# Performance work log

Measured on AMD Instinct MI355X. Metric: run time of the kernel, lower is better.

## Reference

```python
import jax, jax.numpy as jnp
import numpy as np

BLOCK_SIZE = 64  # weights per (scale, zero_point) block along in_features


def _dequant(q_weights, q_scales, q_zp):
    # q_weights: [N, K] int codes in [0,16); q_scales/q_zp: [N, K//BLOCK_SIZE]
    N, K = q_weights.shape
    nb = K // BLOCK_SIZE
    q = q_weights.reshape(N, nb, BLOCK_SIZE).astype(q_scales.dtype)
    zp = q_zp.reshape(N, nb, 1).astype(q_scales.dtype)
    s = q_scales.reshape(N, nb, 1)
    return ((q - zp) * s).reshape(N, K)  # [N, K] float


def setup_inputs() -> dict:
    key = jax.random.key(0)
    k1, k2, k3, k4, k5 = jax.random.split(key, 5)
    M, K, N = 4096, 4096, 11008
    nb = K // BLOCK_SIZE
    return {
        "input": jax.random.normal(k1, (M, K), dtype=jnp.float32),
        "q_weights": jax.random.randint(k2, (N, K), 0, 16, dtype=jnp.int32),
        "q_scales": jax.random.uniform(k3, (N, nb), dtype=jnp.float32, minval=0.01, maxval=0.05),
        "q_zp": jax.random.randint(k4, (N, nb), 0, 16, dtype=jnp.int32),
        "bias": jax.random.normal(k5, (N,), dtype=jnp.float32),
    }


def reference(input, q_weights, q_scales, q_zp, bias):
    # Blockwise int4 dequant + GEMM: out[m, n] = sum_k input[m, k] * w[n, k]
    w = _dequant(q_weights, q_scales, q_zp)          # [N, K]
    out = jnp.einsum("mk,nk->mn", input, w)          # [M, N]
    return out + bias[None, :]
```

## Files before the change

### kernel.cpp

```cpp
#include <hip/hip_runtime.h>


#define BM 128
#define BN 128
#define BK 64
#define LDSN 72

typedef __attribute__((ext_vector_type(8))) short bf16x8;
typedef __attribute__((ext_vector_type(4))) float f32x4;

__device__ __forceinline__ unsigned short f2bf(float f) {
    union { float f; unsigned int u; } v; v.f = f;
    unsigned int u = v.u;
    u += 0x7FFFu + ((u >> 16) & 1u);
    return (unsigned short)(u >> 16);
}
__device__ __forceinline__ unsigned int pack2(float a, float b) {
    return (unsigned int)f2bf(a) | ((unsigned int)f2bf(b) << 16);
}

__device__ __forceinline__ void gl_lds16(const void* gp, void* lp) {
    __builtin_amdgcn_global_load_lds(
        (const __attribute__((address_space(1))) unsigned int*)gp,
        (__attribute__((address_space(3))) unsigned int*)lp,
        16, 0, 0);
}

__device__ __forceinline__ unsigned lds_off(const void* p) {
    return (unsigned)(unsigned long long)
        (const __attribute__((address_space(3))) void*)p;
}

template<int IMM>
__device__ __forceinline__ bf16x8 ds128(unsigned a) {
    bf16x8 d;
    asm volatile("ds_read_b128 %0, %1 offset:%2"
                 : "=v"(d) : "v"(a), "i"(IMM));
    return d;
}

__global__ __launch_bounds__(256)
void prep_kernel(const float* __restrict__ A, const int* __restrict__ Q,
                 const float* __restrict__ S, const int* __restrict__ Zp,
                 unsigned short* __restrict__ Ab, unsigned short* __restrict__ W,
                 int M, int K, int nb)
{
    const int y = blockIdx.y;
    const int k = (blockIdx.x * 256 + threadIdx.x) * 8;
    if (k >= K) return;
    if (y < M) {
        const float4* ap = (const float4*)(A + (size_t)y * K + k);
        float4 a0 = ap[0], a1 = ap[1];
        uint4 o;
        o.x = pack2(a0.x, a0.y); o.y = pack2(a0.z, a0.w);
        o.z = pack2(a1.x, a1.y); o.w = pack2(a1.z, a1.w);
        *(uint4*)(Ab + (size_t)y * K + k) = o;
    } else {
        const int n = y - M;
        const int kb = k >> 6;
        const float s  = S[(size_t)n * nb + kb];
        const float zs = (float)Zp[(size_t)n * nb + kb] * s;
        const int4* qp = (const int4*)(Q + (size_t)n * K + k);
        int4 q0 = qp[0], q1 = qp[1];
        uint4 o;
        o.x = pack2((float)q0.x * s - zs, (float)q0.y * s - zs);
        o.y = pack2((float)q0.z * s - zs, (float)q0.w * s - zs);
        o.z = pack2((float)q1.x * s - zs, (float)q1.y * s - zs);
        o.w = pack2((float)q1.z * s - zs, (float)q1.w * s - zs);
        *(uint4*)(W + (size_t)n * K + k) = o;
    }
}


#define G8_BARRIER() asm volatile("s_barrier" ::: "memory")
#define G8_VMCNT(n)  asm volatile("s_waitcnt vmcnt(" #n ")" ::: "memory")
#define G8_LGKMC(n)  asm volatile("s_waitcnt lgkmcnt(" #n ")" ::: "memory")
#define G8_LGKM0()   do { asm volatile("s_waitcnt lgkmcnt(0)" ::: "memory"); \
    __builtin_amdgcn_sched_barrier(0); } while (0)

#define G8_STAGE(G, kt, h, base, b)                                          \
  do {                                                                       \
    const unsigned short* _s = (G) + (long)(kt) * 64 + (long)(h) * 128 * K;  \
    gl_lds16(_s + aoff0, (base) + (b) * 32768 + (h) * 16384 + lds0);         \
    gl_lds16(_s + aoff1, (base) + (b) * 32768 + (h) * 16384 + lds1);         \
  } while (0)

#define G8_LOAD_AF(b, mh)                                                    \
  af[0][0] = ds128<(b)*32768 + (mh)*16384 + 0*2048>(pA0);                    \
  af[1][0] = ds128<(b)*32768 + (mh)*16384 + 1*2048>(pA0);                    \
  af[2][0] = ds128<(b)*32768 + (mh)*16384 + 2*2048>(pA0);                    \
  af[3][0] = ds128<(b)*32768 + (mh)*16384 + 3*2048>(pA0);                    \
  af[0][1] = ds128<(b)*32768 + (mh)*16384 + 0*2048>(pA1);                    \
  af[1][1] = ds128<(b)*32768 + (mh)*16384 + 1*2048>(pA1);                    \
  af[2][1] = ds128<(b)*32768 + (mh)*16384 + 2*2048>(pA1);                    \
  af[3][1] = ds128<(b)*32768 + (mh)*16384 + 3*2048>(pA1);

#define G8_LOAD_BF(b, nh, BF)                                                \
  BF[0][0] = ds128<(b)*32768 + (nh)*16384 + 0*2048>(pB0);                    \
  BF[1][0] = ds128<(b)*32768 + (nh)*16384 + 1*2048>(pB0);                    \
  BF[0][1] = ds128<(b)*32768 + (nh)*16384 + 0*2048>(pB1);                    \
  BF[1][1] = ds128<(b)*32768 + (nh)*16384 + 1*2048>(pB1);

#define G8_MFMA(q, BF)                                                       \
  __builtin_amdgcn_s_setprio(1);                                             \
  { _Pragma("unroll") for (int _i = 0; _i < 4; ++_i)                         \
    _Pragma("unroll") for (int _j = 0; _j < 2; ++_j) {                       \
      acc[q][_i][_j] = __builtin_amdgcn_mfma_f32_16x16x32_bf16(              \
          af[_i][0], BF[_j][0], acc[q][_i][_j], 0, 0, 0);                    \
      acc[q][_i][_j] = __builtin_amdgcn_mfma_f32_16x16x32_bf16(              \
          af[_i][1], BF[_j][1], acc[q][_i][_j], 0, 0, 0);                    \
  } }                                                                        \
  __builtin_amdgcn_s_setprio(0);

__global__ __launch_bounds__(512, 2)
void gemm8_kernel(const unsigned short* __restrict__ Ab,
                  const unsigned short* __restrict__ Wb,
                  const float* __restrict__ bias, float* __restrict__ C,
                  int M, int N, int K)
{
    __shared__ __align__(16) unsigned short As[2][256][64];
    __shared__ __align__(16) unsigned short Bs[2][256][64];

    const int tid  = threadIdx.x;

    const int nwg = gridDim.x;
    int wg = blockIdx.x;
    {
        const int q8 = nwg >> 3, r8 = nwg & 7, x = wg & 7, s = wg >> 3;
        wg = (x < r8 ? x * (q8 + 1) : r8 * (q8 + 1) + (x - r8) * q8) + s;
    }
    const int gx = M / 256;
    const int m0 = (wg % gx) * 256;
    const int n0 = (wg / gx) * 256;

    const int lane = tid & 63;
    const int wave = tid >> 6;
    const int ww   = wave >> 2;
    const int wv   = wave & 3;
    const int fr   = lane & 15;
    const int quad = lane >> 4;
    const int sw   = fr & 7;

    const int rl0 = tid >> 3;
    const int rl1 = (512 + tid) >> 3;
    const int pp  = tid & 7;
    const long aoff0 = (long)rl0 * K + (long)((pp ^ (rl0 & 7)) * 8);
    const long aoff1 = (long)rl1 * K + (long)((pp ^ (rl1 & 7)) * 8);
    const int lds0 = tid * 16;
    const int lds1 = (512 + tid) * 16;

    const int ck0 = ((quad    ) ^ sw) * 16;
    const int ck1 = ((quad + 4) ^ sw) * 16;
    const int arow = ww * 64 + fr;
    const int brow = wv * 32 + fr;

    char* AsB = (char*)&As[0][0][0];
    char* BsB = (char*)&Bs[0][0][0];
    const unsigned pA0 = lds_off(AsB) + arow * 128 + ck0;
    const unsigned pA1 = lds_off(AsB) + arow * 128 + ck1;
    const unsigned pB0 = lds_off(BsB) + brow * 128 + ck0;
    const unsigned pB1 = lds_off(BsB) + brow * 128 + ck1;

    const unsigned short* Ag = Ab + (size_t)m0 * K;
    const unsigned short* Bg = Wb + (size_t)n0 * K;

    f32x4 acc[4][4][2];
    #pragma unroll
    for (int q = 0; q < 4; ++q)
        #pragma unroll
        for (int i = 0; i < 4; ++i)
            #pragma unroll
            for (int j = 0; j < 2; ++j)
                acc[q][i][j] = (f32x4){0.f, 0.f, 0.f, 0.f};

    bf16x8 af[4][2], bf0[2][2], bf1[2][2];

    G8_STAGE(Ag, 0, 0, AsB, 0);
    G8_STAGE(Bg, 0, 0, BsB, 0);
    G8_STAGE(Ag, 0, 1, AsB, 0);
    G8_STAGE(Bg, 0, 1, BsB, 0);
    G8_STAGE(Ag, 1, 0, AsB, 1);
    G8_STAGE(Bg, 1, 0, BsB, 1);
    G8_VMCNT(4);
    G8_BARRIER();

    const int nit = K / 128;
    for (int it = 0; it < nit - 1; ++it) {
        const int t = 2 * it;
        G8_LOAD_AF(0, 0) G8_LOAD_BF(0, 0, bf0)
        G8_STAGE(Ag, t + 1, 1, AsB, 1);
        G8_LGKMC(8);
        G8_BARRIER(); G8_LGKM0();
        G8_MFMA(0, bf0);
        G8_VMCNT(6);
        G8_BARRIER();
        G8_LOAD_BF(0, 1, bf1)
        G8_STAGE(Bg, t + 1, 1, BsB, 1);
        G8_BARRIER(); G8_LGKM0();
        G8_MFMA(1, bf1);
        G8_BARRIER();
        G8_LOAD_AF(0, 1)
        G8_STAGE(Ag, t + 2, 0, AsB, 0);
        G8_BARRIER(); G8_LGKM0();
        G8_MFMA(2, bf0);
        G8_BARRIER();
        G8_STAGE(Bg, t + 2, 0, BsB, 0);
        G8_BARRIER();
        G8_MFMA(3, bf1);
        G8_VMCNT(8);
        G8_BARRIER();
        G8_LOAD_AF(1, 0) G8_LOAD_BF(1, 0, bf0)
        G8_STAGE(Ag, t + 2, 1, AsB, 0);
        G8_LGKMC(8);
        G8_BARRIER(); G8_LGKM0();
        G8_MFMA(0, bf0);
        G8_VMCNT(6);
        G8_BARRIER();
        G8_LOAD_BF(1, 1, bf1)
        G8_STAGE(Bg, t + 2, 1, BsB, 0);
        G8_BARRIER(); G8_LGKM0();
        G8_MFMA(1, bf1);
        G8_BARRIER();
        G8_LOAD_AF(1, 1)
        G8_STAGE(Ag, t + 3, 0, AsB, 1);
        G8_BARRIER(); G8_LGKM0();
        G8_MFMA(2, bf0);
        G8_BARRIER();
        G8_STAGE(Bg, t + 3, 0, BsB, 1);
        G8_BARRIER();
        G8_MFMA(3, bf1);
        G8_VMCNT(8);
        G8_BARRIER();
    }
    {
        G8_LOAD_AF(0, 0) G8_LOAD_BF(0, 0, bf0)
        G8_STAGE(Ag, 2 * nit - 1, 1, AsB, 1);
        G8_LGKMC(8);
        G8_BARRIER(); G8_LGKM0(); G8_MFMA(0, bf0); G8_VMCNT(6); G8_BARRIER();

        G8_LOAD_BF(0, 1, bf1)
        G8_STAGE(Bg, 2 * nit - 1, 1, BsB, 1);
        G8_BARRIER(); G8_LGKM0(); G8_MFMA(1, bf1); G8_BARRIER();

        G8_LOAD_AF(0, 1)
        G8_BARRIER(); G8_LGKM0(); G8_MFMA(2, bf0); G8_BARRIER();

        G8_BARRIER(); G8_MFMA(3, bf1); G8_VMCNT(4); G8_BARRIER();

        G8_LOAD_AF(1, 0) G8_LOAD_BF(1, 0, bf0)
        G8_BARRIER(); G8_LGKM0(); G8_MFMA(0, bf0); G8_VMCNT(0); G8_BARRIER();

        G8_LOAD_BF(1, 1, bf1)
        G8_BARRIER(); G8_LGKM0(); G8_MFMA(1, bf1); G8_BARRIER();

        G8_LOAD_AF(1, 1)
        G8_BARRIER(); G8_LGKM0(); G8_MFMA(2, bf0); G8_BARRIER();

        G8_MFMA(3, bf1);
    }

    #pragma unroll
    for (int q = 0; q < 4; ++q) {
        const int mh = q >> 1, nh = q & 1;
        #pragma unroll
        for (int j = 0; j < 2; ++j) {
            const int n = n0 + nh * 128 + brow + j * 16;
            const float bv = bias[n];
            #pragma unroll
            for (int i = 0; i < 4; ++i) {
                const int mb = m0 + mh * 128 + ww * 64 + i * 16 + quad * 4;
                #pragma unroll
                for (int r = 0; r < 4; ++r)
                    C[(size_t)(mb + r) * N + n] = acc[q][i][j][r] + bv;
            }
        }
    }
}

__global__ __launch_bounds__(256, 2)
void gemm_bt_kernel(const unsigned short* __restrict__ Ab,
                    const unsigned short* __restrict__ Wb,
                    const float* __restrict__ bias, float* __restrict__ C,
                    int M, int N, int K)
{
    __shared__ __align__(16) unsigned short As[BM * BK];
    __shared__ __align__(16) unsigned short Bs[BN * BK];

    const int tid = threadIdx.x;
    const int m0  = blockIdx.x * BM;
    const int n0  = blockIdx.y * BN;

    const int lane = tid & 63;
    const int wave = tid >> 6;
    const int wm   = (wave >> 1) * 64;
    const int wn   = (wave & 1) * 64;
    const int fr   = lane & 15;
    const int quad = lane >> 4;
    const int sw   = fr & 7;

    f32x4 acc[4][4];
    #pragma unroll
    for (int i = 0; i < 4; ++i)
        #pragma unroll
        for (int j = 0; j < 4; ++j)
            acc[i][j] = (f32x4){0.f, 0.f, 0.f, 0.f};

    const int ktiles = K / BK;
    for (int kt = 0; kt < ktiles; ++kt) {
        const int k0 = kt * BK;
        #pragma unroll
        for (int i = 0; i < 4; ++i) {
            const int c    = i * 256 + tid;
            const int row  = c >> 3;
            const int g    = (c & 7) ^ (row & 7);
            const int cole = g * 8;
            gl_lds16(Ab + (size_t)(m0 + row) * K + k0 + cole, (char*)As + c * 16);
            gl_lds16(Wb + (size_t)(n0 + row) * K + k0 + cole, (char*)Bs + c * 16);
        }
        __syncthreads();

        #pragma unroll
        for (int ks = 0; ks < 2; ++ks) {
            bf16x8 af[4], bfg[4];
            #pragma unroll
            for (int i = 0; i < 4; ++i) {
                const int row = wm + i * 16 + fr;
                const int p   = (ks * 4 + quad) ^ sw;
                af[i] = *(const bf16x8*)&As[row * BK + p * 8];
            }
            #pragma unroll
            for (int j = 0; j < 4; ++j) {
                const int row = wn + j * 16 + fr;
                const int p   = (ks * 4 + quad) ^ sw;
                bfg[j] = *(const bf16x8*)&Bs[row * BK + p * 8];
            }
            #pragma unroll
            for (int i = 0; i < 4; ++i)
                #pragma unroll
                for (int j = 0; j < 4; ++j)
                    acc[i][j] = __builtin_amdgcn_mfma_f32_16x16x32_bf16(af[i], bfg[j], acc[i][j], 0, 0, 0);
        }
        __syncthreads();
    }

    #pragma unroll
    for (int j = 0; j < 4; ++j) {
        const int n = n0 + wn + j * 16 + fr;
        const float bv = bias[n];
        #pragma unroll
        for (int i = 0; i < 4; ++i) {
            const int mb = m0 + wm + i * 16 + quad * 4;
            #pragma unroll
            for (int r = 0; r < 4; ++r)
                C[(size_t)(mb + r) * N + n] = acc[i][j][r] + bv;
        }
    }
}

__global__ __launch_bounds__(256, 2)
void q4gemm_fused(const float* __restrict__ A, const int* __restrict__ Q,
                  const float* __restrict__ S, const int* __restrict__ Zp,
                  const float* __restrict__ bias, float* __restrict__ C,
                  int M, int N, int K, int nb)
{
    __shared__ __align__(16) unsigned short As[BM * LDSN];
    __shared__ __align__(16) unsigned short Bs[BN * LDSN];

    const int tid = threadIdx.x;
    const int m0  = blockIdx.x * BM;
    const int n0  = blockIdx.y * BN;
    const int srow = tid >> 4;
    const int scol = (tid & 15) << 2;
    const int lane = tid & 63;
    const int wave = tid >> 6;
    const int wm   = (wave >> 1) * 64;
    const int wn   = (wave & 1) * 64;
    const int fr   = lane & 15;
    const int quad = lane >> 4;

    f32x4 acc[4][4];
    #pragma unroll
    for (int i = 0; i < 4; ++i)
        #pragma unroll
        for (int j = 0; j < 4; ++j)
            acc[i][j] = (f32x4){0.f, 0.f, 0.f, 0.f};

    const int ktiles = K / BK;
    for (int kt = 0; kt < ktiles; ++kt) {
        const int k0 = kt * BK;
        #pragma unroll
        for (int i = 0; i < 8; ++i) {
            const int r = i * 16 + srow;
            const float4 v = *(const float4*)(A + (size_t)(m0 + r) * K + k0 + scol);
            uint2 p; p.x = pack2(v.x, v.y); p.y = pack2(v.z, v.w);
            *(uint2*)&As[r * LDSN + scol] = p;
        }
        #pragma unroll
        for (int i = 0; i < 8; ++i) {
            const int r = i * 16 + srow;
            const int n = n0 + r;
            const int4 q = *(const int4*)(Q + (size_t)n * K + k0 + scol);
            const float s  = S[(size_t)n * nb + kt];
            const float zs = (float)Zp[(size_t)n * nb + kt] * s;
            uint2 p;
            p.x = pack2((float)q.x * s - zs, (float)q.y * s - zs);
            p.y = pack2((float)q.z * s - zs, (float)q.w * s - zs);
            *(uint2*)&Bs[r * LDSN + scol] = p;
        }
        __syncthreads();
        #pragma unroll
        for (int ks = 0; ks < 2; ++ks) {
            bf16x8 af[4], bfg[4];
            #pragma unroll
            for (int i = 0; i < 4; ++i)
                af[i] = *(const bf16x8*)&As[(wm + i * 16 + fr) * LDSN + ks * 32 + quad * 8];
            #pragma unroll
            for (int j = 0; j < 4; ++j)
                bfg[j] = *(const bf16x8*)&Bs[(wn + j * 16 + fr) * LDSN + ks * 32 + quad * 8];
            #pragma unroll
            for (int i = 0; i < 4; ++i)
                #pragma unroll
                for (int j = 0; j < 4; ++j)
                    acc[i][j] = __builtin_amdgcn_mfma_f32_16x16x32_bf16(af[i], bfg[j], acc[i][j], 0, 0, 0);
        }
        __syncthreads();
    }
    #pragma unroll
    for (int j = 0; j < 4; ++j) {
        const int n = n0 + wn + j * 16 + fr;
        const float bv = bias[n];
        #pragma unroll
        for (int i = 0; i < 4; ++i) {
            const int mb = m0 + wm + i * 16 + quad * 4;
            #pragma unroll
            for (int r = 0; r < 4; ++r)
                C[(size_t)(mb + r) * N + n] = acc[i][j][r] + bv;
        }
    }
}

extern "C" void kernel_launch(void* const* d_in, const int* in_sizes, int n_in,
                              void* d_out, int out_size, void* d_ws, size_t ws_size,
                              hipStream_t stream) {
    const float* A    = (const float*)d_in[0];
    const int*   Q    = (const int*)d_in[1];
    const float* S    = (const float*)d_in[2];
    const int*   Zp   = (const int*)d_in[3];
    const float* bias = (const float*)d_in[4];
    float* C = (float*)d_out;

    const int N  = in_sizes[4];
    const int K  = in_sizes[1] / N;
    const int M  = in_sizes[0] / K;
    const int nb = in_sizes[2] / N;

    const size_t needA = (size_t)M * K * 2;
    const size_t needW = (size_t)N * K * 2;

    if (ws_size >= needA + needW && (K % 2048) == 0) {
        unsigned short* Ab = (unsigned short*)d_ws;
        unsigned short* Wb = (unsigned short*)((char*)d_ws + needA);

        dim3 pgrid(K / 2048, M + N);
        prep_kernel<<<pgrid, 256, 0, stream>>>(A, Q, S, Zp, Ab, Wb, M, K, nb);

        if ((M % 256) == 0 && (N % 256) == 0 && (K % 128) == 0 && K >= 256) {
            gemm8_kernel<<<dim3((M / 256) * (N / 256)), dim3(512), 0, stream>>>(
                Ab, Wb, bias, C, M, N, K);
        } else {
            dim3 grid(M / BM, N / BN);
            gemm_bt_kernel<<<grid, dim3(256), 0, stream>>>(Ab, Wb, bias, C, M, N, K);
        }
    } else {
        dim3 grid(M / BM, N / BN);
        q4gemm_fused<<<grid, dim3(256), 0, stream>>>(A, Q, S, Zp, bias, C, M, N, K, nb);
    }
}
```

Baseline: 654.2 us.

## Double-buffer A fragments and prefetch LDS reads ahead of MFMA phases

Adds a second A-fragment register set so LDS reads for the next quadrant are issued before the current MFMA block runs. Partial lgkmcnt waits replace the full waits and a barrier before each MFMA phase, so LDS latency overlaps with matrix math. The prologue, the main loop and the tail are rescheduled to match, and the launch guard now requires K to be a multiple of 256. The extra fragment registers raise VGPR pressure under the 512-thread, 2-blocks-per-CU launch bound.

```diff
diff --git a/kernel.cpp b/kernel.cpp
--- a/kernel.cpp
+++ b/kernel.cpp
@@ -74,8 +74,7 @@
 
 #define G8_BARRIER() asm volatile("s_barrier" ::: "memory")
 #define G8_VMCNT(n)  asm volatile("s_waitcnt vmcnt(" #n ")" ::: "memory")
-#define G8_LGKMC(n)  asm volatile("s_waitcnt lgkmcnt(" #n ")" ::: "memory")
-#define G8_LGKM0()   do { asm volatile("s_waitcnt lgkmcnt(0)" ::: "memory"); \
+#define G8_LGKMC(n)  do { asm volatile("s_waitcnt lgkmcnt(" #n ")" ::: "memory"); \
     __builtin_amdgcn_sched_barrier(0); } while (0)
 
 #define G8_STAGE(G, kt, h, base, b)                                          \
@@ -85,15 +84,15 @@
     gl_lds16(_s + aoff1, (base) + (b) * 32768 + (h) * 16384 + lds1);         \
   } while (0)
 
-#define G8_LOAD_AF(b, mh)                                                    \
-  af[0][0] = ds128<(b)*32768 + (mh)*16384 + 0*2048>(pA0);                    \
-  af[1][0] = ds128<(b)*32768 + (mh)*16384 + 1*2048>(pA0);                    \
-  af[2][0] = ds128<(b)*32768 + (mh)*16384 + 2*2048>(pA0);                    \
-  af[3][0] = ds128<(b)*32768 + (mh)*16384 + 3*2048>(pA0);                    \
-  af[0][1] = ds128<(b)*32768 + (mh)*16384 + 0*2048>(pA1);                    \
-  af[1][1] = ds128<(b)*32768 + (mh)*16384 + 1*2048>(pA1);                    \
-  af[2][1] = ds128<(b)*32768 + (mh)*16384 + 2*2048>(pA1);                    \
-  af[3][1] = ds128<(b)*32768 + (mh)*16384 + 3*2048>(pA1);
+#define G8_LOAD_AF(b, mh, AF)                                                \
+  AF[0][0] = ds128<(b)*32768 + (mh)*16384 + 0*2048>(pA0);                    \
+  AF[1][0] = ds128<(b)*32768 + (mh)*16384 + 1*2048>(pA0);                    \
+  AF[2][0] = ds128<(b)*32768 + (mh)*16384 + 2*2048>(pA0);                    \
+  AF[3][0] = ds128<(b)*32768 + (mh)*16384 + 3*2048>(pA0);                    \
+  AF[0][1] = ds128<(b)*32768 + (mh)*16384 + 0*2048>(pA1);                    \
+  AF[1][1] = ds128<(b)*32768 + (mh)*16384 + 1*2048>(pA1);                    \
+  AF[2][1] = ds128<(b)*32768 + (mh)*16384 + 2*2048>(pA1);                    \
+  AF[3][1] = ds128<(b)*32768 + (mh)*16384 + 3*2048>(pA1);
 
 #define G8_LOAD_BF(b, nh, BF)                                                \
   BF[0][0] = ds128<(b)*32768 + (nh)*16384 + 0*2048>(pB0);                    \
@@ -101,14 +100,14 @@
   BF[0][1] = ds128<(b)*32768 + (nh)*16384 + 0*2048>(pB1);                    \
   BF[1][1] = ds128<(b)*32768 + (nh)*16384 + 1*2048>(pB1);
 
-#define G8_MFMA(q, BF)                                                       \
+#define G8_MFMA(q, AF, BF)                                                   \
   __builtin_amdgcn_s_setprio(1);                                             \
   { _Pragma("unroll") for (int _i = 0; _i < 4; ++_i)                         \
     _Pragma("unroll") for (int _j = 0; _j < 2; ++_j) {                       \
       acc[q][_i][_j] = __builtin_amdgcn_mfma_f32_16x16x32_bf16(              \
-          af[_i][0], BF[_j][0], acc[q][_i][_j], 0, 0, 0);                    \
+          AF[_i][0], BF[_j][0], acc[q][_i][_j], 0, 0, 0);                    \
       acc[q][_i][_j] = __builtin_amdgcn_mfma_f32_16x16x32_bf16(              \
-          af[_i][1], BF[_j][1], acc[q][_i][_j], 0, 0, 0);                    \
+          AF[_i][1], BF[_j][1], acc[q][_i][_j], 0, 0, 0);                    \
   } }                                                                        \
   __builtin_amdgcn_s_setprio(0);
 
@@ -173,7 +172,7 @@
             for (int j = 0; j < 2; ++j)
                 acc[q][i][j] = (f32x4){0.f, 0.f, 0.f, 0.f};
 
-    bf16x8 af[4][2], bf0[2][2], bf1[2][2];
+    bf16x8 afa[4][2], afb[4][2], bf0[2][2], bf1[2][2];
 
     G8_STAGE(Ag, 0, 0, AsB, 0);
     G8_STAGE(Bg, 0, 0, BsB, 0);
@@ -183,80 +182,84 @@
     G8_STAGE(Bg, 1, 0, BsB, 1);
     G8_VMCNT(4);
     G8_BARRIER();
+    G8_LOAD_AF(0, 0, afa) G8_LOAD_BF(0, 0, bf0)
 
     const int nit = K / 128;
     for (int it = 0; it < nit - 1; ++it) {
         const int t = 2 * it;
-        G8_LOAD_AF(0, 0) G8_LOAD_BF(0, 0, bf0)
+        G8_LOAD_BF(0, 1, bf1)
         G8_STAGE(Ag, t + 1, 1, AsB, 1);
+        G8_LGKMC(4);
+        G8_MFMA(0, afa, bf0);
+        G8_BARRIER();
+        G8_LOAD_AF(0, 1, afb)
+        G8_STAGE(Bg, t + 1, 1, BsB, 1);
         G8_LGKMC(8);
-        G8_BARRIER(); G8_LGKM0();
-        G8_MFMA(0, bf0);
+        G8_MFMA(1, afa, bf1);
+        G8_BARRIER();
+        G8_STAGE(Ag, t + 2, 0, AsB, 0);
+        G8_LGKMC(0);
+        G8_MFMA(2, afb, bf0);
         G8_VMCNT(6);
         G8_BARRIER();
+        G8_LOAD_AF(1, 0, afa) G8_LOAD_BF(1, 0, bf0)
+        G8_STAGE(Bg, t + 2, 0, BsB, 0);
+        G8_MFMA(3, afb, bf1);
+        G8_VMCNT(4);
+        G8_BARRIER();
+        G8_LOAD_BF(1, 1, bf1)
+        G8_STAGE(Ag, t + 2, 1, AsB, 0);
+        G8_LGKMC(4);
+        G8_MFMA(0, afa, bf0);
+        G8_BARRIER();
+        G8_LOAD_AF(1, 1, afb)
+        G8_STAGE(Bg, t + 2, 1, BsB, 0);
+        G8_LGKMC(8);
+        G8_MFMA(1, afa, bf1);
+        G8_BARRIER();
+        G8_STAGE(Ag, t + 3, 0, AsB, 1);
+        G8_LGKMC(0);
+        G8_MFMA(2, afb, bf0);
+        G8_VMCNT(6);
+        G8_BARRIER();
+        G8_LOAD_AF(0, 0, afa) G8_LOAD_BF(0, 0, bf0)
+        G8_STAGE(Bg, t + 3, 0, BsB, 1);
+        G8_MFMA(3, afb, bf1);
+        G8_VMCNT(4);
+        G8_BARRIER();
+    }
+    {
+        const int t = 2 * (nit - 1);
         G8_LOAD_BF(0, 1, bf1)
+        G8_STAGE(Ag, t + 1, 1, AsB, 1);
+        G8_LGKMC(4);
+        G8_MFMA(0, afa, bf0);
+        G8_BARRIER();
+        G8_LOAD_AF(0, 1, afb)
         G8_STAGE(Bg, t + 1, 1, BsB, 1);
-        G8_BARRIER(); G8_LGKM0();
-        G8_MFMA(1, bf1);
-        G8_BARRIER();
-        G8_LOAD_AF(0, 1)
-        G8_STAGE(Ag, t + 2, 0, AsB, 0);
-        G8_BARRIER(); G8_LGKM0();
-        G8_MFMA(2, bf0);
-        G8_BARRIER();
-        G8_STAGE(Bg, t + 2, 0, BsB, 0);
-        G8_BARRIER();
-        G8_MFMA(3, bf1);
-        G8_VMCNT(8);
-        G8_BARRIER();
-        G8_LOAD_AF(1, 0) G8_LOAD_BF(1, 0, bf0)
-        G8_STAGE(Ag, t + 2, 1, AsB, 0);
         G8_LGKMC(8);
-        G8_BARRIER(); G8_LGKM0();
-        G8_MFMA(0, bf0);
-        G8_VMCNT(6);
+        G8_MFMA(1, afa, bf1);
+        G8_BARRIER();
+        G8_LGKMC(0);
+        G8_MFMA(2, afb, bf0);
+        G8_VMCNT(4);
+        G8_BARRIER();
+        G8_LOAD_AF(1, 0, afa) G8_LOAD_BF(1, 0, bf0)
+        G8_MFMA(3, afb, bf1);
+        G8_VMCNT(0);
         G8_BARRIER();
         G8_LOAD_BF(1, 1, bf1)
-        G8_STAGE(Bg, t + 2, 1, BsB, 0);
-        G8_BARRIER(); G8_LGKM0();
-        G8_MFMA(1, bf1);
-        G8_BARRIER();
-        G8_LOAD_AF(1, 1)
-        G8_STAGE(Ag, t + 3, 0, AsB, 1);
-        G8_BARRIER(); G8_LGKM0();
-        G8_MFMA(2, bf0);
-        G8_BARRIER();
-        G8_STAGE(Bg, t + 3, 0, BsB, 1);
-        G8_BARRIER();
-        G8_MFMA(3, bf1);
-        G8_VMCNT(8);
-        G8_BARRIER();
-    }
-    {
-        G8_LOAD_AF(0, 0) G8_LOAD_BF(0, 0, bf0)
-        G8_STAGE(Ag, 2 * nit - 1, 1, AsB, 1);
+        G8_LGKMC(4);
+        G8_MFMA(0, afa, bf0);
+        G8_BARRIER();
+        G8_LOAD_AF(1, 1, afb)
         G8_LGKMC(8);
-        G8_BARRIER(); G8_LGKM0(); G8_MFMA(0, bf0); G8_VMCNT(6); G8_BARRIER();
-
-        G8_LOAD_BF(0, 1, bf1)
-        G8_STAGE(Bg, 2 * nit - 1, 1, BsB, 1);
-        G8_BARRIER(); G8_LGKM0(); G8_MFMA(1, bf1); G8_BARRIER();
-
-        G8_LOAD_AF(0, 1)
-        G8_BARRIER(); G8_LGKM0(); G8_MFMA(2, bf0); G8_BARRIER();
-
-        G8_BARRIER(); G8_MFMA(3, bf1); G8_VMCNT(4); G8_BARRIER();
-
-        G8_LOAD_AF(1, 0) G8_LOAD_BF(1, 0, bf0)
-        G8_BARRIER(); G8_LGKM0(); G8_MFMA(0, bf0); G8_VMCNT(0); G8_BARRIER();
-
-        G8_LOAD_BF(1, 1, bf1)
-        G8_BARRIER(); G8_LGKM0(); G8_MFMA(1, bf1); G8_BARRIER();
-
-        G8_LOAD_AF(1, 1)
-        G8_BARRIER(); G8_LGKM0(); G8_MFMA(2, bf0); G8_BARRIER();
-
-        G8_MFMA(3, bf1);
+        G8_MFMA(1, afa, bf1);
+        G8_BARRIER();
+        G8_LGKMC(0);
+        G8_MFMA(2, afb, bf0);
+        G8_BARRIER();
+        G8_MFMA(3, afb, bf1);
     }
 
     #pragma unroll
@@ -464,7 +467,7 @@
         dim3 pgrid(K / 2048, M + N);
         prep_kernel<<<pgrid, 256, 0, stream>>>(A, Q, S, Zp, Ab, Wb, M, K, nb);
 
-        if ((M % 256) == 0 && (N % 256) == 0 && (K % 128) == 0 && K >= 256) {
+        if ((M % 256) == 0 && (N % 256) == 0 && (K % 256) == 0) {
             gemm8_kernel<<<dim3((M / 256) * (N / 256)), dim3(512), 0, stream>>>(
                 Ab, Wb, bias, C, M, N, K);
         } else {
```

Result: slower. 959.4 us (+46.7%).
